# Kernel optimization log

Hardware: AMD Instinct MI355X
Metric: run time of the kernel (lower is better)

## Reference

```python
import jax, jax.numpy as jnp
import numpy as np

N = 50000   # nodes
E = 800000  # edges (avg degree 16)
D = 128     # input feature dim
H = 128     # hidden_units per FFN layer
BN_EPS = 1e-3  # keras BatchNormalization default epsilon


def setup_inputs() -> dict:
    key = jax.random.key(0)
    ks = jax.random.split(key, 16)
    inp = {}
    inp["node_repr"] = jax.random.normal(ks[0], (N, D), dtype=jnp.float32)
    inp["edges"] = jax.random.randint(ks[1], (2, E), 0, N, dtype=jnp.int32)
    inp["edge_weights"] = jnp.ones((E,), jnp.float32)
    idx = 2
    # ffn_prepare: D -> H -> H ; update_fn: (D+H) -> H -> H
    for pre, dims in [("prep", [(D, H), (H, H)]), ("upd", [(D + H, H), (H, H)])]:
        for li, (din, dout) in enumerate(dims):
            inp[f"{pre}_bn{li}_g"] = jnp.ones((din,), jnp.float32)
            inp[f"{pre}_bn{li}_b"] = jnp.zeros((din,), jnp.float32)
            inp[f"{pre}_bn{li}_m"] = jax.random.normal(ks[idx], (din,), dtype=jnp.float32) * 0.1; idx += 1
            inp[f"{pre}_bn{li}_v"] = jnp.ones((din,), jnp.float32)
            inp[f"{pre}_W{li}"] = jax.random.normal(ks[idx], (din, dout), dtype=jnp.float32) * (din ** -0.5); idx += 1
            inp[f"{pre}_b{li}"] = jnp.zeros((dout,), jnp.float32)
    return inp


def _ffn(x, layers):
    # layers: list of (bn_gamma, bn_beta, bn_mean, bn_var, W, b)
    # each block: BatchNorm (inference) -> Dropout (identity at eval) -> Dense+gelu
    for g, b, m, v, W, bias in layers:
        x = (x - m) * jax.lax.rsqrt(v + BN_EPS) * g + b
        x = jax.nn.gelu(x @ W + bias, approximate=False)
    return x


def reference(node_repr, edges, edge_weights,
              prep_bn0_g, prep_bn0_b, prep_bn0_m, prep_bn0_v, prep_W0, prep_b0,
              prep_bn1_g, prep_bn1_b, prep_bn1_m, prep_bn1_v, prep_W1, prep_b1,
              upd_bn0_g, upd_bn0_b, upd_bn0_m, upd_bn0_v, upd_W0, upd_b0,
              upd_bn1_g, upd_bn1_b, upd_bn1_m, upd_bn1_v, upd_W1, upd_b1):
    node_indices, neighbour_indices = edges[0], edges[1]
    # prepare: gather neighbours, per-edge FFN, scale by edge weight
    nbr = jnp.take(node_repr, neighbour_indices, axis=0)  # [E, D]
    prep_layers = [(prep_bn0_g, prep_bn0_b, prep_bn0_m, prep_bn0_v, prep_W0, prep_b0),
                   (prep_bn1_g, prep_bn1_b, prep_bn1_m, prep_bn1_v, prep_W1, prep_b1)]
    messages = _ffn(nbr, prep_layers) * edge_weights[:, None]  # [E, H]
    # aggregate: unsorted_segment_mean (empty segments -> 0, as in TF)
    ssum = jax.ops.segment_sum(messages, node_indices, num_segments=node_repr.shape[0])
    cnt = jax.ops.segment_sum(jnp.ones((messages.shape[0],), messages.dtype), node_indices,
                              num_segments=node_repr.shape[0])
    agg = jnp.where(cnt[:, None] > 0, ssum / jnp.maximum(cnt, 1.0)[:, None], 0.0)  # [N, H]
    # update: concat + FFN
    h = jnp.concatenate([node_repr, agg], axis=1)  # [N, D+H]
    upd_layers = [(upd_bn0_g, upd_bn0_b, upd_bn0_m, upd_bn0_v, upd_W0, upd_b0),
                  (upd_bn1_g, upd_bn1_b, upd_bn1_m, upd_bn1_v, upd_W1, upd_b1)]
    return _ffn(h, upd_layers)  # [N, H]
```

## Files before the change

### kernel.cpp

```cpp
#include <hip/hip_runtime.h>
#include <math.h>

#define NN 50000
#define NE 800000
#define DD 128
#define HH 128
#define BN_EPS 1e-3f
#define SCB 196

typedef _Float16 f16x8 __attribute__((ext_vector_type(8)));
typedef float f32x4 __attribute__((ext_vector_type(4)));

__device__ __forceinline__ float gelu_f(float x) {
    return 0.5f * x * (1.0f + erff(x * 0.70710678118654752f));
}

struct WArgs {
    const float *W, *g, *bb, *m, *v, *bias;
    _Float16* wt; float* bs; int K;
};

__global__ __launch_bounds__(256)
void weights_all_kernel(WArgs a0, WArgs a1, WArgs a2, WArgs a3)
{
    __shared__ float red[256];
    const int which = blockIdx.x >> 7;
    const int n = blockIdx.x & 127;
    WArgs a = a0;
    if (which == 1) a = a1;
    else if (which == 2) a = a2;
    else if (which == 3) a = a3;
    const int t = threadIdx.x;
    float part = 0.0f;
    for (int k = t; k < a.K; k += 256) {
        float sc = a.g[k] * rsqrtf(a.v[k] + BN_EPS);
        float sh = a.bb[k] - a.m[k] * sc;
        float wv = a.W[(long long)k * HH + n];
        a.wt[(long long)n * a.K + k] = (_Float16)(wv * sc);
        part += sh * wv;
    }
    red[t] = part;
    __syncthreads();
    for (int s = 128; s > 0; s >>= 1) {
        if (t < s) red[t] += red[t + s];
        __syncthreads();
    }
    if (t == 0) a.bs[n] = a.bias[n] + red[0];
}

__global__ __launch_bounds__(256, 4)
void prep_kernel(const float* __restrict__ x,
                 const _Float16* __restrict__ wt0, const float* __restrict__ bs0,
                 const _Float16* __restrict__ wt1, const float* __restrict__ bs1,
                 _Float16* __restrict__ msg, _Float16* __restrict__ xh)
{
    __shared__ __align__(16) _Float16 smem[32 * DD];
    const int tid = threadIdx.x;
    const int w = tid >> 6, lane = tid & 63;
    const int row0 = blockIdx.x * 32;
    const int cl = lane & 15;
    const int kg = lane >> 4;

    f16x8 b0[4][2];
#pragma unroll
    for (int kc = 0; kc < 4; ++kc)
#pragma unroll
        for (int ct = 0; ct < 2; ++ct) {
            int col = w * 32 + ct * 16 + cl;
            b0[kc][ct] = *reinterpret_cast<const f16x8*>(&wt0[(long long)col * DD + kc * 32 + kg * 8]);
        }

    for (int i = tid; i < 32 * (DD / 8); i += 256) {
        int r = i >> 4, k8 = i & 15;
        int row = row0 + r;
        f16x8 h;
        if (row < NN) {
            const float4* p = reinterpret_cast<const float4*>(&x[(long long)row * DD + k8 * 8]);
            float4 u0 = p[0], u1 = p[1];
            h[0] = (_Float16)u0.x; h[1] = (_Float16)u0.y; h[2] = (_Float16)u0.z; h[3] = (_Float16)u0.w;
            h[4] = (_Float16)u1.x; h[5] = (_Float16)u1.y; h[6] = (_Float16)u1.z; h[7] = (_Float16)u1.w;
            *reinterpret_cast<f16x8*>(&xh[(long long)row * DD + k8 * 8]) = h;
        } else {
#pragma unroll
            for (int q = 0; q < 8; ++q) h[q] = (_Float16)0.0f;
        }
        int slot = (r * 16 + k8) ^ (r & 7);
        *reinterpret_cast<f16x8*>(&smem[slot * 8]) = h;
    }
    __syncthreads();

    const f32x4 zero = {0.0f, 0.0f, 0.0f, 0.0f};
    f32x4 acc[2][2];
#pragma unroll
    for (int rt = 0; rt < 2; ++rt)
#pragma unroll
        for (int ct = 0; ct < 2; ++ct) acc[rt][ct] = zero;

#pragma unroll
    for (int kc = 0; kc < 4; ++kc) {
        int k8 = kc * 4 + kg;
#pragma unroll
        for (int rt = 0; rt < 2; ++rt) {
            int rA = rt * 16 + cl;
            int slot = (rA * 16 + k8) ^ (rA & 7);
            f16x8 a = *reinterpret_cast<const f16x8*>(&smem[slot * 8]);
#pragma unroll
            for (int ct = 0; ct < 2; ++ct)
                acc[rt][ct] = __builtin_amdgcn_mfma_f32_16x16x32_f16(a, b0[kc][ct], acc[rt][ct], 0, 0, 0);
        }
    }

    f16x8 b1[4][2];
#pragma unroll
    for (int kc = 0; kc < 4; ++kc)
#pragma unroll
        for (int ct = 0; ct < 2; ++ct) {
            int col = w * 32 + ct * 16 + cl;
            b1[kc][ct] = *reinterpret_cast<const f16x8*>(&wt1[(long long)col * HH + kc * 32 + kg * 8]);
        }

    __syncthreads();

#pragma unroll
    for (int ct = 0; ct < 2; ++ct) {
        int col = w * 32 + ct * 16 + cl;
        float bias = bs0[col];
#pragma unroll
        for (int rt = 0; rt < 2; ++rt)
#pragma unroll
            for (int rr = 0; rr < 4; ++rr) {
                int r = rt * 16 + kg * 4 + rr;
                float vv = gelu_f(acc[rt][ct][rr] + bias);
                int slot = (r * 16 + (col >> 3)) ^ (r & 7);
                smem[slot * 8 + (col & 7)] = (_Float16)vv;
            }
    }
    __syncthreads();

    f32x4 acc2[2][2];
#pragma unroll
    for (int rt = 0; rt < 2; ++rt)
#pragma unroll
        for (int ct = 0; ct < 2; ++ct) acc2[rt][ct] = zero;

#pragma unroll
    for (int kc = 0; kc < 4; ++kc) {
        int k8 = kc * 4 + kg;
#pragma unroll
        for (int rt = 0; rt < 2; ++rt) {
            int rA = rt * 16 + cl;
            int slot = (rA * 16 + k8) ^ (rA & 7);
            f16x8 a = *reinterpret_cast<const f16x8*>(&smem[slot * 8]);
#pragma unroll
            for (int ct = 0; ct < 2; ++ct)
                acc2[rt][ct] = __builtin_amdgcn_mfma_f32_16x16x32_f16(a, b1[kc][ct], acc2[rt][ct], 0, 0, 0);
        }
    }

#pragma unroll
    for (int ct = 0; ct < 2; ++ct) {
        int col = w * 32 + ct * 16 + cl;
        float bias = bs1[col];
#pragma unroll
        for (int rt = 0; rt < 2; ++rt)
#pragma unroll
            for (int rr = 0; rr < 4; ++rr) {
                int row = row0 + rt * 16 + kg * 4 + rr;
                if (row < NN)
                    msg[(long long)row * HH + col] = (_Float16)gelu_f(acc2[rt][ct][rr] + bias);
            }
    }
}

__global__ __launch_bounds__(256)
void degpos_kernel(const int* __restrict__ edges, int* __restrict__ deg,
                   int* __restrict__ pos)
{
    int e = blockIdx.x * 256 + threadIdx.x;
    if (e < NE) pos[e] = atomicAdd(&deg[edges[e]], 1);
}

__global__ __launch_bounds__(256)
void scan_partial_kernel(const int* __restrict__ deg, int* __restrict__ part)
{
    __shared__ int red[256];
    int t = threadIdx.x;
    int i = blockIdx.x * 256 + t;
    red[t] = (i < NN) ? deg[i] : 0;
    __syncthreads();
    for (int s = 128; s > 0; s >>= 1) {
        if (t < s) red[t] += red[t + s];
        __syncthreads();
    }
    if (t == 0) part[blockIdx.x] = red[0];
}

__global__ __launch_bounds__(256)
void scan_offsets_kernel(const int* __restrict__ part, int* __restrict__ boff)
{
    __shared__ int s[256];
    int t = threadIdx.x;
    s[t] = (t < SCB) ? part[t] : 0;
    __syncthreads();
    for (int off = 1; off < 256; off <<= 1) {
        int v = (t >= off) ? s[t - off] : 0;
        __syncthreads();
        s[t] += v;
        __syncthreads();
    }
    boff[t] = (t == 0) ? 0 : s[t - 1];
}

__global__ __launch_bounds__(256)
void scan_write_kernel(const int* __restrict__ deg, const int* __restrict__ boff,
                       int* __restrict__ rowptr)
{
    __shared__ int s[256];
    int t = threadIdx.x, b = blockIdx.x;
    int i = b * 256 + t;
    int v = (i < NN) ? deg[i] : 0;
    s[t] = v;
    __syncthreads();
    for (int off = 1; off < 256; off <<= 1) {
        int u = (t >= off) ? s[t - off] : 0;
        __syncthreads();
        s[t] += u;
        __syncthreads();
    }
    if (i < NN) rowptr[i] = boff[b] + (s[t] - v);
    if (b == SCB - 1 && t == 255) rowptr[NN] = boff[b] + s[255];
}

__global__ __launch_bounds__(256)
void fill_kernel(const int* __restrict__ edges, const float* __restrict__ ew,
                 const int* __restrict__ rowptr, const int* __restrict__ pos,
                 int2* __restrict__ rec)
{
    int e = blockIdx.x * 256 + threadIdx.x;
    if (e >= NE) return;
    int d = edges[e];
    int idx = rowptr[d] + pos[e];
    int2 r;
    r.x = edges[NE + e];
    r.y = __float_as_int(ew[e]);
    rec[idx] = r;
}

__global__ __launch_bounds__(256)
void gather_kernel(const int* __restrict__ rowptr, const int2* __restrict__ rec,
                   const _Float16* __restrict__ msg, _Float16* __restrict__ aggh)
{
    int gwave = (blockIdx.x * 256 + threadIdx.x) >> 6;
    int lane = threadIdx.x & 63;
    int sub = lane >> 4, l16 = lane & 15;
    int node = gwave * 4 + sub;
    if (node >= NN) return;
    int beg = rowptr[node], end = rowptr[node + 1];
    float acc[8];
#pragma unroll
    for (int q = 0; q < 8; ++q) acc[q] = 0.0f;
    for (int j = beg; j < end; ++j) {
        int2 rc = rec[j];
        int src = rc.x;
        float w = __int_as_float(rc.y);
        f16x8 m = *reinterpret_cast<const f16x8*>(&msg[(long long)src * HH + l16 * 8]);
#pragma unroll
        for (int q = 0; q < 8; ++q) acc[q] += (float)m[q] * w;
    }
    float inv = (end > beg) ? 1.0f / (float)(end - beg) : 0.0f;
    f16x8 o;
#pragma unroll
    for (int q = 0; q < 8; ++q) o[q] = (_Float16)(acc[q] * inv);
    *reinterpret_cast<f16x8*>(&aggh[(long long)node * HH + l16 * 8]) = o;
}

__global__ __launch_bounds__(256, 4)
void upd_kernel(const _Float16* __restrict__ xh, const _Float16* __restrict__ aggh,
                const _Float16* __restrict__ wt2, const float* __restrict__ bs2,
                const _Float16* __restrict__ wt3, const float* __restrict__ bs3,
                float* __restrict__ out)
{
    const int KK = DD + HH;
    __shared__ __align__(16) _Float16 smem[32 * 256];
    const int tid = threadIdx.x;
    const int w = tid >> 6, lane = tid & 63;
    const int row0 = blockIdx.x * 32;
    const int cl = lane & 15;
    const int kg = lane >> 4;

    f16x8 b0[8][2];
#pragma unroll
    for (int kc = 0; kc < 8; ++kc)
#pragma unroll
        for (int ct = 0; ct < 2; ++ct) {
            int col = w * 32 + ct * 16 + cl;
            b0[kc][ct] = *reinterpret_cast<const f16x8*>(&wt2[(long long)col * 256 + kc * 32 + kg * 8]);
        }

    for (int i = tid; i < 32 * (KK / 8); i += 256) {
        int r = i >> 5, k8 = i & 31;
        int row = row0 + r;
        f16x8 h;
        if (row < NN) {
            if (k8 < 16) {
                h = *reinterpret_cast<const f16x8*>(&xh[(long long)row * DD + k8 * 8]);
            } else {
                h = *reinterpret_cast<const f16x8*>(&aggh[(long long)row * HH + (k8 - 16) * 8]);
            }
        } else {
#pragma unroll
            for (int q = 0; q < 8; ++q) h[q] = (_Float16)0.0f;
        }
        int slot = (r * 32 + k8) ^ (r & 7);
        *reinterpret_cast<f16x8*>(&smem[slot * 8]) = h;
    }
    __syncthreads();

    const f32x4 zero = {0.0f, 0.0f, 0.0f, 0.0f};
    f32x4 acc[2][2];
#pragma unroll
    for (int rt = 0; rt < 2; ++rt)
#pragma unroll
        for (int ct = 0; ct < 2; ++ct) acc[rt][ct] = zero;

#pragma unroll
    for (int kc = 0; kc < 8; ++kc) {
        int k8 = kc * 4 + kg;
#pragma unroll
        for (int rt = 0; rt < 2; ++rt) {
            int rA = rt * 16 + cl;
            int slot = (rA * 32 + k8) ^ (rA & 7);
            f16x8 a = *reinterpret_cast<const f16x8*>(&smem[slot * 8]);
#pragma unroll
            for (int ct = 0; ct < 2; ++ct)
                acc[rt][ct] = __builtin_amdgcn_mfma_f32_16x16x32_f16(a, b0[kc][ct], acc[rt][ct], 0, 0, 0);
        }
    }

    f16x8 b1[4][2];
#pragma unroll
    for (int kc = 0; kc < 4; ++kc)
#pragma unroll
        for (int ct = 0; ct < 2; ++ct) {
            int col = w * 32 + ct * 16 + cl;
            b1[kc][ct] = *reinterpret_cast<const f16x8*>(&wt3[(long long)col * HH + kc * 32 + kg * 8]);
        }

    __syncthreads();

#pragma unroll
    for (int ct = 0; ct < 2; ++ct) {
        int col = w * 32 + ct * 16 + cl;
        float bias = bs2[col];
#pragma unroll
        for (int rt = 0; rt < 2; ++rt)
#pragma unroll
            for (int rr = 0; rr < 4; ++rr) {
                int r = rt * 16 + kg * 4 + rr;
                float vv = gelu_f(acc[rt][ct][rr] + bias);
                int slot = (r * 16 + (col >> 3)) ^ (r & 7);
                smem[slot * 8 + (col & 7)] = (_Float16)vv;
            }
    }
    __syncthreads();

    f32x4 acc2[2][2];
#pragma unroll
    for (int rt = 0; rt < 2; ++rt)
#pragma unroll
        for (int ct = 0; ct < 2; ++ct) acc2[rt][ct] = zero;

#pragma unroll
    for (int kc = 0; kc < 4; ++kc) {
        int k8 = kc * 4 + kg;
#pragma unroll
        for (int rt = 0; rt < 2; ++rt) {
            int rA = rt * 16 + cl;
            int slot = (rA * 16 + k8) ^ (rA & 7);
            f16x8 a = *reinterpret_cast<const f16x8*>(&smem[slot * 8]);
#pragma unroll
            for (int ct = 0; ct < 2; ++ct)
                acc2[rt][ct] = __builtin_amdgcn_mfma_f32_16x16x32_f16(a, b1[kc][ct], acc2[rt][ct], 0, 0, 0);
        }
    }

#pragma unroll
    for (int ct = 0; ct < 2; ++ct) {
        int col = w * 32 + ct * 16 + cl;
        float bias = bs3[col];
#pragma unroll
        for (int rt = 0; rt < 2; ++rt)
#pragma unroll
            for (int rr = 0; rr < 4; ++rr) {
                int row = row0 + rt * 16 + kg * 4 + rr;
                if (row < NN)
                    out[(long long)row * HH + col] = gelu_f(acc2[rt][ct][rr] + bias);
            }
    }
}

extern "C" void kernel_launch(void* const* d_in, const int* in_sizes, int n_in,
                              void* d_out, int out_size, void* d_ws, size_t ws_size,
                              hipStream_t stream) {
    const float* node_repr = (const float*)d_in[0];
    const int*   edges     = (const int*)d_in[1];
    const float* ew        = (const float*)d_in[2];

    const float* prep_bn0_g = (const float*)d_in[3];
    const float* prep_bn0_b = (const float*)d_in[4];
    const float* prep_bn0_m = (const float*)d_in[5];
    const float* prep_bn0_v = (const float*)d_in[6];
    const float* prep_W0    = (const float*)d_in[7];
    const float* prep_b0    = (const float*)d_in[8];
    const float* prep_bn1_g = (const float*)d_in[9];
    const float* prep_bn1_b = (const float*)d_in[10];
    const float* prep_bn1_m = (const float*)d_in[11];
    const float* prep_bn1_v = (const float*)d_in[12];
    const float* prep_W1    = (const float*)d_in[13];
    const float* prep_b1    = (const float*)d_in[14];

    const float* upd_bn0_g = (const float*)d_in[15];
    const float* upd_bn0_b = (const float*)d_in[16];
    const float* upd_bn0_m = (const float*)d_in[17];
    const float* upd_bn0_v = (const float*)d_in[18];
    const float* upd_W0    = (const float*)d_in[19];
    const float* upd_b0    = (const float*)d_in[20];
    const float* upd_bn1_g = (const float*)d_in[21];
    const float* upd_bn1_b = (const float*)d_in[22];
    const float* upd_bn1_m = (const float*)d_in[23];
    const float* upd_bn1_v = (const float*)d_in[24];
    const float* upd_W1    = (const float*)d_in[25];
    const float* upd_b1    = (const float*)d_in[26];

    _Float16* msg  = (_Float16*)d_ws;
    _Float16* aggh = msg + (size_t)NN * HH;
    _Float16* xh   = aggh + (size_t)NN * HH;
    _Float16* wt0  = xh + (size_t)NN * DD;
    _Float16* wt1  = wt0 + 128 * 128;
    _Float16* wt2  = wt1 + 128 * 128;
    _Float16* wt3  = wt2 + 128 * 256;
    float* bs0 = (float*)(wt3 + 128 * 128);
    float* bs1 = bs0 + 128;
    float* bs2 = bs1 + 128;
    float* bs3 = bs2 + 128;
    int* deg    = (int*)(bs3 + 128);
    int* rowptr = deg + NN;
    int* part   = rowptr + NN + 1;
    int* boff   = part + 256;
    int* pos    = boff + 256;
    int2* rec   = (int2*)(pos + NE);

    hipMemsetAsync(deg, 0, (size_t)NN * sizeof(int), stream);

    WArgs a0 = {prep_W0, prep_bn0_g, prep_bn0_b, prep_bn0_m, prep_bn0_v, prep_b0, wt0, bs0, DD};
    WArgs a1 = {prep_W1, prep_bn1_g, prep_bn1_b, prep_bn1_m, prep_bn1_v, prep_b1, wt1, bs1, HH};
    WArgs a2 = {upd_W0, upd_bn0_g, upd_bn0_b, upd_bn0_m, upd_bn0_v, upd_b0, wt2, bs2, DD + HH};
    WArgs a3 = {upd_W1, upd_bn1_g, upd_bn1_b, upd_bn1_m, upd_bn1_v, upd_b1, wt3, bs3, HH};
    weights_all_kernel<<<512, 256, 0, stream>>>(a0, a1, a2, a3);

    int nblk = (NN + 31) / 32;
    prep_kernel<<<nblk, 256, 0, stream>>>(node_repr, wt0, bs0, wt1, bs1, msg, xh);

    int eblk = (NE + 255) / 256;
    degpos_kernel<<<eblk, 256, 0, stream>>>(edges, deg, pos);
    scan_partial_kernel<<<SCB, 256, 0, stream>>>(deg, part);
    scan_offsets_kernel<<<1, 256, 0, stream>>>(part, boff);
    scan_write_kernel<<<SCB, 256, 0, stream>>>(deg, boff, rowptr);
    fill_kernel<<<eblk, 256, 0, stream>>>(edges, ew, rowptr, pos, rec);

    int gblk = (NN + 15) / 16;
    gather_kernel<<<gblk, 256, 0, stream>>>(rowptr, rec, msg, aggh);

    upd_kernel<<<nblk, 256, 0, stream>>>(xh, aggh, wt2, bs2, wt3, bs3,
                                         (float*)d_out);
}
```

Baseline: 175.2 us.

## Merge independent launches and load MFMA A-operands directly from global memory

Weight folding and degree counting now share one launch, and the per-node prep FFN shares a launch with the CSR fill, so independent work runs side by side and there are fewer kernel boundaries. The prep and update kernels no longer stage input rows in shared memory. Each lane loads its fp32 A-fragment straight from node_repr and converts it to half in registers, which removes the fp16 copy xh, a write/read round trip and one barrier. In exchange the global loads are strided per lane rather than staged and coalesced, and node_repr is read twice.

```diff
diff --git a/kernel.cpp b/kernel.cpp
--- a/kernel.cpp
+++ b/kernel.cpp
@@ -7,6 +7,9 @@
 #define HH 128
 #define BN_EPS 1e-3f
 #define SCB 196
+#define PBLK 1563
+#define EBLK 3125
+#define WBLK 512
 
 typedef _Float16 f16x8 __attribute__((ext_vector_type(8)));
 typedef float f32x4 __attribute__((ext_vector_type(4)));
@@ -21,8 +24,15 @@
 };
 
 __global__ __launch_bounds__(256)
-void weights_all_kernel(WArgs a0, WArgs a1, WArgs a2, WArgs a3)
-{
+void wdeg_kernel(WArgs a0, WArgs a1, WArgs a2, WArgs a3,
+                 const int* __restrict__ edges, int* __restrict__ deg,
+                 int* __restrict__ pos)
+{
+    if (blockIdx.x >= WBLK) {
+        int e = (blockIdx.x - WBLK) * 256 + threadIdx.x;
+        if (e < NE) pos[e] = atomicAdd(&deg[edges[e]], 1);
+        return;
+    }
     __shared__ float red[256];
     const int which = blockIdx.x >> 7;
     const int n = blockIdx.x & 127;
@@ -48,13 +58,79 @@
     if (t == 0) a.bs[n] = a.bias[n] + red[0];
 }
 
+__global__ __launch_bounds__(256)
+void scan_partial_kernel(const int* __restrict__ deg, int* __restrict__ part)
+{
+    __shared__ int red[256];
+    int t = threadIdx.x;
+    int i = blockIdx.x * 256 + t;
+    red[t] = (i < NN) ? deg[i] : 0;
+    __syncthreads();
+    for (int s = 128; s > 0; s >>= 1) {
+        if (t < s) red[t] += red[t + s];
+        __syncthreads();
+    }
+    if (t == 0) part[blockIdx.x] = red[0];
+}
+
+__global__ __launch_bounds__(256)
+void scan_offsets_kernel(const int* __restrict__ part, int* __restrict__ boff)
+{
+    __shared__ int s[256];
+    int t = threadIdx.x;
+    s[t] = (t < SCB) ? part[t] : 0;
+    __syncthreads();
+    for (int off = 1; off < 256; off <<= 1) {
+        int v = (t >= off) ? s[t - off] : 0;
+        __syncthreads();
+        s[t] += v;
+        __syncthreads();
+    }
+    boff[t] = (t == 0) ? 0 : s[t - 1];
+}
+
+__global__ __launch_bounds__(256)
+void scan_write_kernel(const int* __restrict__ deg, const int* __restrict__ boff,
+                       int* __restrict__ rowptr)
+{
+    __shared__ int s[256];
+    int t = threadIdx.x, b = blockIdx.x;
+    int i = b * 256 + t;
+    int v = (i < NN) ? deg[i] : 0;
+    s[t] = v;
+    __syncthreads();
+    for (int off = 1; off < 256; off <<= 1) {
+        int u = (t >= off) ? s[t - off] : 0;
+        __syncthreads();
+        s[t] += u;
+        __syncthreads();
+    }
+    if (i < NN) rowptr[i] = boff[b] + (s[t] - v);
+    if (b == SCB - 1 && t == 255) rowptr[NN] = boff[b] + s[255];
+}
+
 __global__ __launch_bounds__(256, 4)
-void prep_kernel(const float* __restrict__ x,
-                 const _Float16* __restrict__ wt0, const float* __restrict__ bs0,
-                 const _Float16* __restrict__ wt1, const float* __restrict__ bs1,
-                 _Float16* __restrict__ msg, _Float16* __restrict__ xh)
-{
-    __shared__ __align__(16) _Float16 smem[32 * DD];
+void prep_fill_kernel(const float* __restrict__ x,
+                      const _Float16* __restrict__ wt0, const float* __restrict__ bs0,
+                      const _Float16* __restrict__ wt1, const float* __restrict__ bs1,
+                      _Float16* __restrict__ msg,
+                      const int* __restrict__ edges, const float* __restrict__ ew,
+                      const int* __restrict__ rowptr, const int* __restrict__ pos,
+                      int2* __restrict__ rec)
+{
+    __shared__ __align__(16) _Float16 ys[32 * HH];
+    if (blockIdx.x >= PBLK) {
+        int e = (blockIdx.x - PBLK) * 256 + threadIdx.x;
+        if (e < NE) {
+            int d = edges[e];
+            int idx = rowptr[d] + pos[e];
+            int2 r;
+            r.x = edges[NE + e];
+            r.y = __float_as_int(ew[e]);
+            rec[idx] = r;
+        }
+        return;
+    }
     const int tid = threadIdx.x;
     const int w = tid >> 6, lane = tid & 63;
     const int row0 = blockIdx.x * 32;
@@ -70,25 +146,6 @@
             b0[kc][ct] = *reinterpret_cast<const f16x8*>(&wt0[(long long)col * DD + kc * 32 + kg * 8]);
         }
 
-    for (int i = tid; i < 32 * (DD / 8); i += 256) {
-        int r = i >> 4, k8 = i & 15;
-        int row = row0 + r;
-        f16x8 h;
-        if (row < NN) {
-            const float4* p = reinterpret_cast<const float4*>(&x[(long long)row * DD + k8 * 8]);
-            float4 u0 = p[0], u1 = p[1];
-            h[0] = (_Float16)u0.x; h[1] = (_Float16)u0.y; h[2] = (_Float16)u0.z; h[3] = (_Float16)u0.w;
-            h[4] = (_Float16)u1.x; h[5] = (_Float16)u1.y; h[6] = (_Float16)u1.z; h[7] = (_Float16)u1.w;
-            *reinterpret_cast<f16x8*>(&xh[(long long)row * DD + k8 * 8]) = h;
-        } else {
-#pragma unroll
-            for (int q = 0; q < 8; ++q) h[q] = (_Float16)0.0f;
-        }
-        int slot = (r * 16 + k8) ^ (r & 7);
-        *reinterpret_cast<f16x8*>(&smem[slot * 8]) = h;
-    }
-    __syncthreads();
-
     const f32x4 zero = {0.0f, 0.0f, 0.0f, 0.0f};
     f32x4 acc[2][2];
 #pragma unroll
@@ -98,12 +155,15 @@
 
 #pragma unroll
     for (int kc = 0; kc < 4; ++kc) {
-        int k8 = kc * 4 + kg;
 #pragma unroll
         for (int rt = 0; rt < 2; ++rt) {
-            int rA = rt * 16 + cl;
-            int slot = (rA * 16 + k8) ^ (rA & 7);
-            f16x8 a = *reinterpret_cast<const f16x8*>(&smem[slot * 8]);
+            int row = row0 + rt * 16 + cl;
+            if (row >= NN) row = NN - 1;
+            const float4* p = reinterpret_cast<const float4*>(&x[(long long)row * DD + kc * 32 + kg * 8]);
+            float4 u0 = p[0], u1 = p[1];
+            f16x8 a;
+            a[0] = (_Float16)u0.x; a[1] = (_Float16)u0.y; a[2] = (_Float16)u0.z; a[3] = (_Float16)u0.w;
+            a[4] = (_Float16)u1.x; a[5] = (_Float16)u1.y; a[6] = (_Float16)u1.z; a[7] = (_Float16)u1.w;
 #pragma unroll
             for (int ct = 0; ct < 2; ++ct)
                 acc[rt][ct] = __builtin_amdgcn_mfma_f32_16x16x32_f16(a, b0[kc][ct], acc[rt][ct], 0, 0, 0);
@@ -118,8 +178,6 @@
             int col = w * 32 + ct * 16 + cl;
             b1[kc][ct] = *reinterpret_cast<const f16x8*>(&wt1[(long long)col * HH + kc * 32 + kg * 8]);
         }
-
-    __syncthreads();
 
 #pragma unroll
     for (int ct = 0; ct < 2; ++ct) {
@@ -132,7 +190,7 @@
                 int r = rt * 16 + kg * 4 + rr;
                 float vv = gelu_f(acc[rt][ct][rr] + bias);
                 int slot = (r * 16 + (col >> 3)) ^ (r & 7);
-                smem[slot * 8 + (col & 7)] = (_Float16)vv;
+                ys[slot * 8 + (col & 7)] = (_Float16)vv;
             }
     }
     __syncthreads();
@@ -150,7 +208,7 @@
         for (int rt = 0; rt < 2; ++rt) {
             int rA = rt * 16 + cl;
             int slot = (rA * 16 + k8) ^ (rA & 7);
-            f16x8 a = *reinterpret_cast<const f16x8*>(&smem[slot * 8]);
+            f16x8 a = *reinterpret_cast<const f16x8*>(&ys[slot * 8]);
 #pragma unroll
             for (int ct = 0; ct < 2; ++ct)
                 acc2[rt][ct] = __builtin_amdgcn_mfma_f32_16x16x32_f16(a, b1[kc][ct], acc2[rt][ct], 0, 0, 0);
@@ -170,80 +228,6 @@
                     msg[(long long)row * HH + col] = (_Float16)gelu_f(acc2[rt][ct][rr] + bias);
             }
     }
-}
-
-__global__ __launch_bounds__(256)
-void degpos_kernel(const int* __restrict__ edges, int* __restrict__ deg,
-                   int* __restrict__ pos)
-{
-    int e = blockIdx.x * 256 + threadIdx.x;
-    if (e < NE) pos[e] = atomicAdd(&deg[edges[e]], 1);
-}
-
-__global__ __launch_bounds__(256)
-void scan_partial_kernel(const int* __restrict__ deg, int* __restrict__ part)
-{
-    __shared__ int red[256];
-    int t = threadIdx.x;
-    int i = blockIdx.x * 256 + t;
-    red[t] = (i < NN) ? deg[i] : 0;
-    __syncthreads();
-    for (int s = 128; s > 0; s >>= 1) {
-        if (t < s) red[t] += red[t + s];
-        __syncthreads();
-    }
-    if (t == 0) part[blockIdx.x] = red[0];
-}
-
-__global__ __launch_bounds__(256)
-void scan_offsets_kernel(const int* __restrict__ part, int* __restrict__ boff)
-{
-    __shared__ int s[256];
-    int t = threadIdx.x;
-    s[t] = (t < SCB) ? part[t] : 0;
-    __syncthreads();
-    for (int off = 1; off < 256; off <<= 1) {
-        int v = (t >= off) ? s[t - off] : 0;
-        __syncthreads();
-        s[t] += v;
-        __syncthreads();
-    }
-    boff[t] = (t == 0) ? 0 : s[t - 1];
-}
-
-__global__ __launch_bounds__(256)
-void scan_write_kernel(const int* __restrict__ deg, const int* __restrict__ boff,
-                       int* __restrict__ rowptr)
-{
-    __shared__ int s[256];
-    int t = threadIdx.x, b = blockIdx.x;
-    int i = b * 256 + t;
-    int v = (i < NN) ? deg[i] : 0;
-    s[t] = v;
-    __syncthreads();
-    for (int off = 1; off < 256; off <<= 1) {
-        int u = (t >= off) ? s[t - off] : 0;
-        __syncthreads();
-        s[t] += u;
-        __syncthreads();
-    }
-    if (i < NN) rowptr[i] = boff[b] + (s[t] - v);
-    if (b == SCB - 1 && t == 255) rowptr[NN] = boff[b] + s[255];
-}
-
-__global__ __launch_bounds__(256)
-void fill_kernel(const int* __restrict__ edges, const float* __restrict__ ew,
-                 const int* __restrict__ rowptr, const int* __restrict__ pos,
-                 int2* __restrict__ rec)
-{
-    int e = blockIdx.x * 256 + threadIdx.x;
-    if (e >= NE) return;
-    int d = edges[e];
-    int idx = rowptr[d] + pos[e];
-    int2 r;
-    r.x = edges[NE + e];
-    r.y = __float_as_int(ew[e]);
-    rec[idx] = r;
 }
 
 __global__ __launch_bounds__(256)
@@ -275,13 +259,12 @@
 }
 
 __global__ __launch_bounds__(256, 4)
-void upd_kernel(const _Float16* __restrict__ xh, const _Float16* __restrict__ aggh,
+void upd_kernel(const float* __restrict__ x, const _Float16* __restrict__ aggh,
                 const _Float16* __restrict__ wt2, const float* __restrict__ bs2,
                 const _Float16* __restrict__ wt3, const float* __restrict__ bs3,
                 float* __restrict__ out)
 {
-    const int KK = DD + HH;
-    __shared__ __align__(16) _Float16 smem[32 * 256];
+    __shared__ __align__(16) _Float16 ys[32 * HH];
     const int tid = threadIdx.x;
     const int w = tid >> 6, lane = tid & 63;
     const int row0 = blockIdx.x * 32;
@@ -297,25 +280,6 @@
             b0[kc][ct] = *reinterpret_cast<const f16x8*>(&wt2[(long long)col * 256 + kc * 32 + kg * 8]);
         }
 
-    for (int i = tid; i < 32 * (KK / 8); i += 256) {
-        int r = i >> 5, k8 = i & 31;
-        int row = row0 + r;
-        f16x8 h;
-        if (row < NN) {
-            if (k8 < 16) {
-                h = *reinterpret_cast<const f16x8*>(&xh[(long long)row * DD + k8 * 8]);
-            } else {
-                h = *reinterpret_cast<const f16x8*>(&aggh[(long long)row * HH + (k8 - 16) * 8]);
-            }
-        } else {
-#pragma unroll
-            for (int q = 0; q < 8; ++q) h[q] = (_Float16)0.0f;
-        }
-        int slot = (r * 32 + k8) ^ (r & 7);
-        *reinterpret_cast<f16x8*>(&smem[slot * 8]) = h;
-    }
-    __syncthreads();
-
     const f32x4 zero = {0.0f, 0.0f, 0.0f, 0.0f};
     f32x4 acc[2][2];
 #pragma unroll
@@ -325,12 +289,19 @@
 
 #pragma unroll
     for (int kc = 0; kc < 8; ++kc) {
-        int k8 = kc * 4 + kg;
 #pragma unroll
         for (int rt = 0; rt < 2; ++rt) {
-            int rA = rt * 16 + cl;
-            int slot = (rA * 32 + k8) ^ (rA & 7);
-            f16x8 a = *reinterpret_cast<const f16x8*>(&smem[slot * 8]);
+            int row = row0 + rt * 16 + cl;
+            if (row >= NN) row = NN - 1;
+            f16x8 a;
+            if (kc < 4) {
+                const float4* p = reinterpret_cast<const float4*>(&x[(long long)row * DD + kc * 32 + kg * 8]);
+                float4 u0 = p[0], u1 = p[1];
+                a[0] = (_Float16)u0.x; a[1] = (_Float16)u0.y; a[2] = (_Float16)u0.z; a[3] = (_Float16)u0.w;
+                a[4] = (_Float16)u1.x; a[5] = (_Float16)u1.y; a[6] = (_Float16)u1.z; a[7] = (_Float16)u1.w;
+            } else {
+                a = *reinterpret_cast<const f16x8*>(&aggh[(long long)row * HH + (kc - 4) * 32 + kg * 8]);
+            }
 #pragma unroll
             for (int ct = 0; ct < 2; ++ct)
                 acc[rt][ct] = __builtin_amdgcn_mfma_f32_16x16x32_f16(a, b0[kc][ct], acc[rt][ct], 0, 0, 0);
@@ -345,8 +316,6 @@
             int col = w * 32 + ct * 16 + cl;
             b1[kc][ct] = *reinterpret_cast<const f16x8*>(&wt3[(long long)col * HH + kc * 32 + kg * 8]);
         }
-
-    __syncthreads();
 
 #pragma unroll
     for (int ct = 0; ct < 2; ++ct) {
@@ -359,7 +328,7 @@
                 int r = rt * 16 + kg * 4 + rr;
                 float vv = gelu_f(acc[rt][ct][rr] + bias);
                 int slot = (r * 16 + (col >> 3)) ^ (r & 7);
-                smem[slot * 8 + (col & 7)] = (_Float16)vv;
+                ys[slot * 8 + (col & 7)] = (_Float16)vv;
             }
     }
     __syncthreads();
@@ -377,7 +346,7 @@
         for (int rt = 0; rt < 2; ++rt) {
             int rA = rt * 16 + cl;
             int slot = (rA * 16 + k8) ^ (rA & 7);
-            f16x8 a = *reinterpret_cast<const f16x8*>(&smem[slot * 8]);
+            f16x8 a = *reinterpret_cast<const f16x8*>(&ys[slot * 8]);
 #pragma unroll
             for (int ct = 0; ct < 2; ++ct)
                 acc2[rt][ct] = __builtin_amdgcn_mfma_f32_16x16x32_f16(a, b1[kc][ct], acc2[rt][ct], 0, 0, 0);
@@ -434,8 +403,7 @@
 
     _Float16* msg  = (_Float16*)d_ws;
     _Float16* aggh = msg + (size_t)NN * HH;
-    _Float16* xh   = aggh + (size_t)NN * HH;
-    _Float16* wt0  = xh + (size_t)NN * DD;
+    _Float16* wt0  = aggh + (size_t)NN * HH;
     _Float16* wt1  = wt0 + 128 * 128;
     _Float16* wt2  = wt1 + 128 * 128;
     _Float16* wt3  = wt2 + 128 * 256;
@@ -456,21 +424,19 @@
     WArgs a1 = {prep_W1, prep_bn1_g, prep_bn1_b, prep_bn1_m, prep_bn1_v, prep_b1, wt1, bs1, HH};
     WArgs a2 = {upd_W0, upd_bn0_g, upd_bn0_b, upd_bn0_m, upd_bn0_v, upd_b0, wt2, bs2, DD + HH};
     WArgs a3 = {upd_W1, upd_bn1_g, upd_bn1_b, upd_bn1_m, upd_bn1_v, upd_b1, wt3, bs3, HH};
-    weights_all_kernel<<<512, 256, 0, stream>>>(a0, a1, a2, a3);
-
-    int nblk = (NN + 31) / 32;
-    prep_kernel<<<nblk, 256, 0, stream>>>(node_repr, wt0, bs0, wt1, bs1, msg, xh);
-
-    int eblk = (NE + 255) / 256;
-    degpos_kernel<<<eblk, 256, 0, stream>>>(edges, deg, pos);
+
+    wdeg_kernel<<<WBLK + EBLK, 256, 0, stream>>>(a0, a1, a2, a3, edges, deg, pos);
+
     scan_partial_kernel<<<SCB, 256, 0, stream>>>(deg, part);
     scan_offsets_kernel<<<1, 256, 0, stream>>>(part, boff);
     scan_write_kernel<<<SCB, 256, 0, stream>>>(deg, boff, rowptr);
-    fill_kernel<<<eblk, 256, 0, stream>>>(edges, ew, rowptr, pos, rec);
+
+    prep_fill_kernel<<<PBLK + EBLK, 256, 0, stream>>>(node_repr, wt0, bs0, wt1, bs1,
+                                                      msg, edges, ew, rowptr, pos, rec);
 
     int gblk = (NN + 15) / 16;
     gather_kernel<<<gblk, 256, 0, stream>>>(rowptr, rec, msg, aggh);
 
-    upd_kernel<<<nblk, 256, 0, stream>>>(xh, aggh, wt2, bs2, wt3, bs3,
+    upd_kernel<<<PBLK, 256, 0, stream>>>(node_repr, aggh, wt2, bs2, wt3, bs3,
                                          (float*)d_out);
 }
```

Result: slower. 178.7 us (+2.0%).
